# Kernel optimization log

Measured on AMD Instinct MI355X. Metric: run time of the kernel, lower is better.

The kernel has to match this reference:

```python
import jax, jax.numpy as jnp
import numpy as np

BIT = 64
NUM_TRAIN = 100000
N_CLASS = 100
BATCH = 128
MU = 1.0
NU = 0.1
ETA = 55.0
DCC_ITER = 10


def setup_inputs() -> dict:
    key = jax.random.key(0)
    k1, k2, k3, k4, k5 = jax.random.split(key, 5)
    u = jax.random.normal(k1, (BATCH, BIT), dtype=jnp.float32)
    y = (jax.random.uniform(k2, (BATCH, N_CLASS)) < 0.1).astype(jnp.float32)
    ind = jnp.arange(BATCH, dtype=jnp.int32)  # unique column indices into num_train
    U = jax.random.normal(k3, (BIT, NUM_TRAIN), dtype=jnp.float32)
    B = jnp.sign(jax.random.normal(k4, (BIT, NUM_TRAIN), dtype=jnp.float32))  # +-1 codes
    Ybuf = (jax.random.uniform(k5, (N_CLASS, NUM_TRAIN)) < 0.1).astype(jnp.float32)
    return {"u": u, "y": y, "ind": ind, "U": U, "B": B, "Ybuf": Ybuf}


def _update_b_and_w(B, U, Ybuf):
    # Faithful DCC: dcc_iter outer iterations; within each, W from a ridge
    # solve, then sequential sign coordinate-descent over the `bit` rows of B.
    lam_eye = (NU / MU) * jnp.eye(BIT, dtype=B.dtype)
    W = None
    for _ in range(DCC_ITER):
        # W = inv(B B^T + (nu/mu) I) @ B @ Y^T  -> (bit, n_class)
        W = jnp.linalg.solve(B @ B.T + lam_eye, B @ Ybuf.T)
        P = W @ Ybuf + (ETA / MU) * U  # (bit, num_train); constant within inner loop

        def body(Bc, i):
            w = W[i]                         # (n_class,)
            Ww = W @ w                       # (bit,)
            # B_prime.T @ W_prime @ w == B.T @ (W @ w) - B[i] * (w . w)
            row = jnp.sign(P[i] - (Ww @ Bc - Bc[i] * (w @ w)))
            return Bc.at[i].set(row), None

        B, _ = jax.lax.scan(body, B, jnp.arange(BIT))
    return B, W


def reference(u, y, ind, U, B, Ybuf):
    # buffer updates: U gets detached u (torch uses u.t().data), Y gets y
    U = U.at[:, ind].set(jax.lax.stop_gradient(u).T)
    Ybuf = Ybuf.at[:, ind].set(y.T)
    B, W = _update_b_and_w(B, U, Ybuf)

    inner_product = (u @ U) * 0.5                       # (batch, num_train)
    s = (y @ Ybuf > 0).astype(u.dtype)                  # (batch, num_train)
    likelihood = jnp.log1p(jnp.exp(-jnp.abs(inner_product))) \
        + jnp.maximum(inner_product, 0.0) - s * inner_product
    likelihood_loss = jnp.mean(likelihood)
    cl_loss = jnp.mean((y.T - W.T @ B[:, ind]) ** 2)    # (n_class, batch)
    reg_loss = jnp.mean(W ** 2)
    return likelihood_loss + MU * cl_loss + NU * reg_loss
```

## Files before the change

kernel.cpp:

```cpp
#include <hip/hip_runtime.h>
#include <cstdint>
#include <cstddef>


#define NT 100000
#define WPR 1568
#define NWREAL 1563
#define NGRPP 1568
#define NJB 1563
#define ETA_MU 55.0f
#define LAM 0.1f

typedef unsigned long long u64;
typedef _Float16 half8 __attribute__((ext_vector_type(8)));
typedef _Float16 half4 __attribute__((ext_vector_type(4)));
typedef _Float16 half2v __attribute__((ext_vector_type(2)));
typedef float float4v __attribute__((ext_vector_type(4)));

__device__ inline float hsum8(half8 a) {
  half4 lo = __builtin_shufflevector(a, a, 0, 1, 2, 3);
  half4 hi = __builtin_shufflevector(a, a, 4, 5, 6, 7);
  half4 s4 = lo + hi;
  half2v l2 = __builtin_shufflevector(s4, s4, 0, 1);
  half2v h2 = __builtin_shufflevector(s4, s4, 2, 3);
  half2v s2 = l2 + h2;
  return (float)s2[0] + (float)s2[1];
}

__device__ inline u64 transpose64(u64 x, int lane) {
  const u64 ms[6] = {0x5555555555555555ull,0x3333333333333333ull,0x0F0F0F0F0F0F0F0Full,
                     0x00FF00FF00FF00FFull,0x0000FFFF0000FFFFull,0x00000000FFFFFFFFull};
#pragma unroll
  for (int si = 0; si < 6; ++si) {
    int s = 1 << si;
    u64 m = ms[si];
    u64 y = __shfl_xor(x, s, 64);
    if ((lane & s) == 0) x = (x & m) | ((y & m) << s);
    else                 x = (x & ~m) | ((y & ~m) >> s);
  }
  return x;
}

__device__ inline int wave_reduce_i32(int v) {
#pragma unroll
  for (int off = 32; off > 0; off >>= 1) v += __shfl_down(v, off, 64);
  return v;
}
__device__ inline double wave_reduce_f64(double v) {
#pragma unroll
  for (int off = 32; off > 0; off >>= 1) v += __shfl_down(v, off, 64);
  return v;
}

__global__ __launch_bounds__(256) void build_colmasks(
    const float* __restrict__ B, const float* __restrict__ Ybuf,
    u64* __restrict__ Bmask, u64* __restrict__ Ymask,
    signed char* __restrict__ owner, int* __restrict__ cflags) {
  if (blockIdx.x == 0 && threadIdx.x < 16) cflags[threadIdx.x] = 0;
  int j0 = (blockIdx.x * 256 + threadIdx.x) * 4;
  if (j0 >= NT) return;
  *(int*)&owner[j0] = -1;
  u64 bm[4] = {0, 0, 0, 0};
#pragma unroll
  for (int i = 0; i < 64; ++i) {
    float4 v = *(const float4*)&B[(size_t)i * NT + j0];
    bm[0] |= ((u64)(v.x > 0.0f)) << i;
    bm[1] |= ((u64)(v.y > 0.0f)) << i;
    bm[2] |= ((u64)(v.z > 0.0f)) << i;
    bm[3] |= ((u64)(v.w > 0.0f)) << i;
  }
  u64 m0[4] = {0, 0, 0, 0}, m1[4] = {0, 0, 0, 0};
#pragma unroll
  for (int c = 0; c < 100; ++c) {
    float4 v = *(const float4*)&Ybuf[(size_t)c * NT + j0];
    if (c < 64) {
      m0[0] |= ((u64)(v.x > 0.5f)) << c;
      m0[1] |= ((u64)(v.y > 0.5f)) << c;
      m0[2] |= ((u64)(v.z > 0.5f)) << c;
      m0[3] |= ((u64)(v.w > 0.5f)) << c;
    } else {
      m1[0] |= ((u64)(v.x > 0.5f)) << (c - 64);
      m1[1] |= ((u64)(v.y > 0.5f)) << (c - 64);
      m1[2] |= ((u64)(v.z > 0.5f)) << (c - 64);
      m1[3] |= ((u64)(v.w > 0.5f)) << (c - 64);
    }
  }
#pragma unroll
  for (int t = 0; t < 4; ++t) {
    Bmask[j0 + t] = bm[t];
    Ymask[2 * (j0 + t)] = m0[t];
    Ymask[2 * (j0 + t) + 1] = m1[t];
  }
}

__global__ void scatter_y(const float* __restrict__ y, const int* __restrict__ ind,
                          u64* __restrict__ Ymask, u64* __restrict__ ybatch,
                          signed char* __restrict__ owner) {
  int b = threadIdx.x;
  if (b >= 128) return;
  u64 m0 = 0, m1 = 0;
  for (int c = 0; c < 100; ++c) {
    bool v = y[b * 100 + c] > 0.5f;
    if (c < 64) m0 |= ((u64)v) << c;
    else        m1 |= ((u64)v) << (c - 64);
  }
  ybatch[2 * b] = m0;
  ybatch[2 * b + 1] = m1;
  int col = ind[b];
  Ymask[2 * col] = m0;
  Ymask[2 * col + 1] = m1;
  owner[col] = (signed char)b;
}

__global__ __launch_bounds__(256) void build_rows(
    const u64* __restrict__ Bmask, const u64* __restrict__ Ymask,
    u64* __restrict__ Brow, u64* __restrict__ Yrow) {
  int g = blockIdx.x * 4 + (threadIdx.x >> 6);
  int lane = threadIdx.x & 63;
  if (g >= NGRPP) return;
  int j = g * 64 + lane;
  bool act = j < NT;
  u64 bm = act ? Bmask[j] : 0ull;
  u64 y0 = act ? Ymask[2 * j] : 0ull;
  u64 y1 = act ? Ymask[2 * j + 1] : 0ull;
  u64 tb = transpose64(bm, lane);
  Brow[(size_t)lane * WPR + g] = tb;
  u64 t0 = transpose64(y0, lane);
  Yrow[(size_t)lane * WPR + g] = t0;
  u64 t1 = transpose64(y1, lane);
  if (lane < 36) Yrow[(size_t)(64 + lane) * WPR + g] = t1;
}

__global__ __launch_bounds__(256) void popcY_k(const u64* __restrict__ Yrow,
                                               int* __restrict__ popcY) {
  int c = blockIdx.x;
  __shared__ int red[4];
  int s = 0;
  for (int w = threadIdx.x; w < NWREAL; w += 256)
    s += __popcll(Yrow[(size_t)c * WPR + w]);
  s = wave_reduce_i32(s);
  if ((threadIdx.x & 63) == 0) red[threadIdx.x >> 6] = s;
  __syncthreads();
  if (threadIdx.x == 0) popcY[c] = red[0] + red[1] + red[2] + red[3];
}

__global__ __launch_bounds__(256, 4) void k1_sr(
    const u64* __restrict__ Brow, const u64* __restrict__ Yrow,
    int* __restrict__ S_part, int* __restrict__ R_part,
    int it, const int* __restrict__ cflags) {
  if (it > 0 && cflags[it - 1] == 0) return;
  int k = blockIdx.x;
  int q = blockIdx.y;
  int w0 = q * 196;
  int wv = threadIdx.x >> 6, lane = threadIdx.x & 63;
  u64 tmask = (lane < 4) ? ~0ull : 0ull;
  const u64* bk = Brow + (size_t)k * WPR + w0;
  u64 b0 = bk[lane], b1 = bk[lane + 64], b2 = bk[lane + 128];
  u64 b3 = bk[192 + (lane & 3)] & tmask;
  int sS[16];
#pragma unroll
  for (int m = 0; m < 16; ++m) {
    const u64* br = Brow + (size_t)(4 * m + wv) * WPR + w0;
    u64 x0 = br[lane], x1 = br[lane + 64], x2 = br[lane + 128];
    u64 x3 = br[192 + (lane & 3)] & tmask;
    sS[m] = __popcll(x0 ^ b0) + __popcll(x1 ^ b1) +
            __popcll(x2 ^ b2) + __popcll(x3 ^ b3);
  }
  int sR[25];
#pragma unroll
  for (int m = 0; m < 25; ++m) {
    const u64* yr = Yrow + (size_t)(4 * m + wv) * WPR + w0;
    u64 x0 = yr[lane], x1 = yr[lane + 64], x2 = yr[lane + 128];
    u64 x3 = yr[192 + (lane & 3)] & tmask;
    sR[m] = __popcll(x0 & b0) + __popcll(x1 & b1) +
            __popcll(x2 & b2) + __popcll(x3 & b3);
  }
#pragma unroll
  for (int off = 32; off > 0; off >>= 1) {
#pragma unroll
    for (int m = 0; m < 16; ++m) sS[m] += __shfl_down(sS[m], off, 64);
#pragma unroll
    for (int m = 0; m < 25; ++m) sR[m] += __shfl_down(sR[m], off, 64);
  }
  if (lane == 0) {
#pragma unroll
    for (int m = 0; m < 16; ++m)
      S_part[q * 4096 + k * 64 + 4 * m + wv] = sS[m];
#pragma unroll
    for (int m = 0; m < 25; ++m)
      R_part[q * 6400 + k * 100 + 4 * m + wv] = sR[m];
  }
}

__global__ __launch_bounds__(256, 1) void k2a_solve(
    const int* __restrict__ S_part, const int* __restrict__ R_part,
    const int* __restrict__ popcY, float* __restrict__ Wr,
    float* __restrict__ Wc, int it, const int* __restrict__ cflags) {
  if (it > 0 && cflags[it - 1] == 0) return;
  __shared__ short sEi[4096];
  __shared__ _Float16 sXa[64 * 32];
  __shared__ _Float16 sXb[64 * 32];
  int tid = threadIdx.x;
  int wv = tid >> 6, k = tid & 63;
  int b = blockIdx.x;
  const int qbase_t[4] = {0, 7, 14, 20};
  const int qcnt_t[4]  = {7, 7, 6, 6};
  int qbase = qbase_t[b], Q = qcnt_t[b];
  const int off7[4] = {0, 2, 4, 6}, cnt7[4] = {2, 2, 2, 1};
  const int off6[4] = {0, 2, 4, 5}, cnt6[4] = {2, 2, 1, 1};
  int woff = (Q == 7) ? off7[wv] : off6[wv];
  int wcnt = (Q == 7) ? cnt7[wv] : cnt6[wv];
  const float alpha = 1.0f / (100000.0f + LAM);
  for (int e = tid; e < 4096; e += 256) {
    int kk = e >> 6, ll = e & 63;
    int mm = 0;
#pragma unroll
    for (int qq = 0; qq < 8; ++qq) mm += S_part[qq * 4096 + e];
    int v = (kk == ll) ? 0 : (NT - 2 * mm);
    v = v > 32767 ? 32767 : (v < -32767 ? -32767 : v);
    sEi[kk * 64 + (ll ^ (kk & 31))] = (short)v;
  }
  float4 rr4[2], xf[2];
#pragma unroll
  for (int q = 0; q < 2; ++q) {
    if (q < wcnt) {
      float tmp[4];
#pragma unroll
      for (int e4 = 0; e4 < 4; ++e4) {
        int cg = 4 * (qbase + woff + q) + e4;
        float rv = 0.0f;
        if (cg < 100) {
          int rr = 0;
#pragma unroll
          for (int qq = 0; qq < 8; ++qq) rr += R_part[qq * 6400 + k * 100 + cg];
          rv = (float)(2 * rr - popcY[cg]);
        }
        tmp[e4] = rv;
      }
      rr4[q] = make_float4(tmp[0], tmp[1], tmp[2], tmp[3]);
      xf[q] = make_float4(alpha * tmp[0], alpha * tmp[1],
                          alpha * tmp[2], alpha * tmp[3]);
    }
  }
  if (wcnt == 2) {
    half8 h;
    h[0] = (_Float16)xf[0].x; h[1] = (_Float16)xf[0].y;
    h[2] = (_Float16)xf[0].z; h[3] = (_Float16)xf[0].w;
    h[4] = (_Float16)xf[1].x; h[5] = (_Float16)xf[1].y;
    h[6] = (_Float16)xf[1].z; h[7] = (_Float16)xf[1].w;
    *(half8*)&sXa[k * 32 + 4 * woff] = h;
  } else {
    half4 h;
    h[0] = (_Float16)xf[0].x; h[1] = (_Float16)xf[0].y;
    h[2] = (_Float16)xf[0].z; h[3] = (_Float16)xf[0].w;
    *(half4*)&sXa[k * 32 + 4 * woff] = h;
  }
  __syncthreads();
  _Float16* Xs = sXa;
  _Float16* Xd = sXb;
  for (int it2 = 0; it2 < 4; ++it2) {
    float4 a4[2];
#pragma unroll
    for (int q = 0; q < 2; ++q)
      if (q < wcnt) a4[q] = rr4[q];
    if (wcnt == 2) {
      for (int l = 0; l < 64; ++l) {
        float ev = (float)sEi[k * 64 + (l ^ (k & 31))];
        half8 x8 = *(const half8*)&Xs[l * 32 + 4 * woff];
        a4[0].x -= ev * (float)x8[0]; a4[0].y -= ev * (float)x8[1];
        a4[0].z -= ev * (float)x8[2]; a4[0].w -= ev * (float)x8[3];
        a4[1].x -= ev * (float)x8[4]; a4[1].y -= ev * (float)x8[5];
        a4[1].z -= ev * (float)x8[6]; a4[1].w -= ev * (float)x8[7];
      }
    } else {
      for (int l = 0; l < 64; ++l) {
        float ev = (float)sEi[k * 64 + (l ^ (k & 31))];
        half4 x4 = *(const half4*)&Xs[l * 32 + 4 * woff];
        a4[0].x -= ev * (float)x4[0]; a4[0].y -= ev * (float)x4[1];
        a4[0].z -= ev * (float)x4[2]; a4[0].w -= ev * (float)x4[3];
      }
    }
#pragma unroll
    for (int q = 0; q < 2; ++q) {
      if (q < wcnt) {
        xf[q] = make_float4(alpha * a4[q].x, alpha * a4[q].y,
                            alpha * a4[q].z, alpha * a4[q].w);
      }
    }
    if (it2 < 3) {
      if (wcnt == 2) {
        half8 h;
        h[0] = (_Float16)xf[0].x; h[1] = (_Float16)xf[0].y;
        h[2] = (_Float16)xf[0].z; h[3] = (_Float16)xf[0].w;
        h[4] = (_Float16)xf[1].x; h[5] = (_Float16)xf[1].y;
        h[6] = (_Float16)xf[1].z; h[7] = (_Float16)xf[1].w;
        *(half8*)&Xd[k * 32 + 4 * woff] = h;
      } else {
        half4 h;
        h[0] = (_Float16)xf[0].x; h[1] = (_Float16)xf[0].y;
        h[2] = (_Float16)xf[0].z; h[3] = (_Float16)xf[0].w;
        *(half4*)&Xd[k * 32 + 4 * woff] = h;
      }
      __syncthreads();
      _Float16* t = Xs; Xs = Xd; Xd = t;
    }
  }
#pragma unroll
  for (int q = 0; q < 2; ++q) {
    if (q < wcnt) {
      float v4[4] = {xf[q].x, xf[q].y, xf[q].z, xf[q].w};
#pragma unroll
      for (int e4 = 0; e4 < 4; ++e4) {
        int cg = 4 * (qbase + woff + q) + e4;
        if (cg < 100) {
          Wr[k * 100 + cg] = v4[e4];
          Wc[cg * 64 + k] = v4[e4];
        }
      }
    }
  }
}

__global__ __launch_bounds__(256, 1) void k2b_gram(
    const float* __restrict__ Wr, float* __restrict__ G,
    int it, const int* __restrict__ cflags) {
  if (it > 0 && cflags[it - 1] == 0) return;
  __shared__ float sX[6400];
  int tid = threadIdx.x, wv = tid >> 6, k = tid & 63;
  for (int t = tid; t < 6400; t += 256) sX[t] = Wr[t];
  __syncthreads();
  float4 xl[25];
#pragma unroll
  for (int q = 0; q < 25; ++q) xl[q] = *(const float4*)&sX[k * 100 + 4 * q];
#pragma unroll
  for (int ii = 0; ii < 4; ++ii) {
    int i = blockIdx.x * 16 + wv * 4 + ii;
    const float4* xi = (const float4*)&sX[i * 100];
    float d0 = 0.f, d1 = 0.f, d2 = 0.f, d3 = 0.f;
#pragma unroll
    for (int q = 0; q < 25; ++q) {
      float4 a = xi[q];
      d0 += xl[q].x * a.x; d1 += xl[q].y * a.y;
      d2 += xl[q].z * a.z; d3 += xl[q].w * a.w;
    }
    G[i * 64 + k] = (d0 + d1) + (d2 + d3);
  }
}

__global__ __launch_bounds__(256, 2) void k3_gs(
    const float* __restrict__ U, const float* __restrict__ u,
    const signed char* __restrict__ owner, const float* __restrict__ Wc,
    const float* __restrict__ Gm, u64* __restrict__ Bmask,
    u64* __restrict__ Brow, const u64* __restrict__ Ymask,
    int it, int* __restrict__ cflags) {
  if (it > 0 && cflags[it - 1] == 0) return;
  __shared__ _Float16 sWh[100 * 72];
  __shared__ _Float16 sGh[64 * 64];
  __shared__ float sGd[64];
  for (int t = threadIdx.x; t < 6400; t += 256) {
    int c = t >> 6, i = t & 63;
    sWh[c * 72 + i] = (_Float16)Wc[t];
  }
  for (int t = threadIdx.x; t < 4096; t += 256) sGh[t] = (_Float16)Gm[t];
  if (threadIdx.x < 64) sGd[threadIdx.x] = Gm[threadIdx.x * 65];
  __syncthreads();
  int g = blockIdx.x * 4 + (threadIdx.x >> 6);
  int lane = threadIdx.x & 63;
  int j = g * 64 + lane;
  bool act = j < NT;
  int jc = act ? j : NT - 1;
  int ow = owner[jc];
  float p[64];
  if (ow >= 0) {
#pragma unroll
    for (int i = 0; i < 64; ++i) p[i] = ETA_MU * u[ow * 64 + i];
  } else {
#pragma unroll
    for (int i = 0; i < 64; ++i) p[i] = ETA_MU * U[(size_t)i * NT + jc];
  }
  u64 y0 = Ymask[2 * jc], y1 = Ymask[2 * jc + 1];
  half8 pw[8];
#pragma unroll
  for (int t = 0; t < 8; ++t) pw[t] = (half8)(_Float16)0.0f;
  u64 mm = y0;
  while (mm) {
    int c = __builtin_ctzll(mm); mm &= mm - 1;
    const half8* wr = (const half8*)&sWh[c * 72];
#pragma unroll
    for (int t = 0; t < 8; ++t) pw[t] += wr[t];
  }
  mm = y1;
  while (mm) {
    int c = 64 + __builtin_ctzll(mm); mm &= mm - 1;
    const half8* wr = (const half8*)&sWh[c * 72];
#pragma unroll
    for (int t = 0; t < 8; ++t) pw[t] += wr[t];
  }
#pragma unroll
  for (int t = 0; t < 8; ++t)
#pragma unroll
    for (int e = 0; e < 8; ++e)
      p[8 * t + e] += (float)pw[t][e];
  u64 bm = Bmask[jc];
  half8 bfh[8];
#pragma unroll
  for (int t = 0; t < 8; ++t)
#pragma unroll
    for (int e = 0; e < 8; ++e)
      bfh[t][e] = ((bm >> (8 * t + e)) & 1ull) ? (_Float16)1.0f : (_Float16)-1.0f;
#pragma unroll
  for (int i = 0; i < 64; ++i) {
    const half8* gr = (const half8*)&sGh[i * 64];
    half8 d = gr[0] * bfh[0];
#pragma unroll
    for (int t = 1; t < 8; ++t) d += gr[t] * bfh[t];
    float dot = hsum8(d);
    float bfi = (float)bfh[i >> 3][i & 7];
    float val = p[i] - dot + sGd[i] * bfi;
    bfh[i >> 3][i & 7] = (val > 0.0f) ? (_Float16)1.0f : (_Float16)-1.0f;
  }
  u64 nm = 0;
#pragma unroll
  for (int t = 0; t < 8; ++t)
#pragma unroll
    for (int e = 0; e < 8; ++e)
      if (bfh[t][e] > (_Float16)0.0f) nm |= 1ull << (8 * t + e);
  if (!act) nm = 0;
  bool ch = act && (nm != bm);
  if (__any(ch) && lane == 0) cflags[it] = 1;
  if (act) Bmask[j] = nm;
  u64 tb = transpose64(nm, lane);
  Brow[(size_t)lane * WPR + g] = tb;
}

__global__ __launch_bounds__(256, 4) void l1_like(
    const float* __restrict__ U, const float* __restrict__ u,
    const signed char* __restrict__ owner, const u64* __restrict__ Ymask,
    const u64* __restrict__ ybatch, double* __restrict__ partial) {
  __shared__ _Float16 shu[8192];
  __shared__ u64 sy[256];
  __shared__ double wred[4];
  int tid = threadIdx.x;
  for (int e = tid; e < 1024; e += 256) {
    int b = e >> 3, k8 = e & 7;
    const float4* src = (const float4*)&u[b * 64 + k8 * 8];
    float4 f0 = src[0], f1 = src[1];
    half8 h;
    h[0] = (_Float16)f0.x; h[1] = (_Float16)f0.y;
    h[2] = (_Float16)f0.z; h[3] = (_Float16)f0.w;
    h[4] = (_Float16)f1.x; h[5] = (_Float16)f1.y;
    h[6] = (_Float16)f1.z; h[7] = (_Float16)f1.w;
    *(half8*)&shu[b * 64 + ((k8 ^ (b & 7)) * 8)] = h;
  }
  if (tid < 256) sy[tid] = ybatch[tid];
  __syncthreads();
  int wv = tid >> 6, lane = tid & 63;
  int n = lane & 15, q = lane >> 4;
  int j = blockIdx.x * 64 + wv * 16 + n;
  bool actj = j < NT;
  int jc = actj ? j : NT - 1;
  int ow = owner[jc];
  half8 bf0, bf1;
#pragma unroll
  for (int t = 0; t < 8; ++t) {
    int k = q * 8 + t;
    bf0[t] = (_Float16)U[(size_t)k * NT + jc];
    bf1[t] = (_Float16)U[(size_t)(k + 32) * NT + jc];
  }
  if (ow >= 0) {
#pragma unroll
    for (int t = 0; t < 8; ++t) {
      bf0[t] = (_Float16)u[ow * 64 + q * 8 + t];
      bf1[t] = (_Float16)u[ow * 64 + 32 + q * 8 + t];
    }
  }
  u64 ym0 = Ymask[2 * jc], ym1 = Ymask[2 * jc + 1];
  float lsum = 0.0f;
#pragma unroll
  for (int t8 = 0; t8 < 8; ++t8) {
    int brow = t8 * 16 + n;
    half8 a0 = *(const half8*)&shu[brow * 64 + ((q ^ (brow & 7)) * 8)];
    half8 a1 = *(const half8*)&shu[brow * 64 + (((q + 4) ^ (brow & 7)) * 8)];
    float4v c = {0.f, 0.f, 0.f, 0.f};
    c = __builtin_amdgcn_mfma_f32_16x16x32_f16(a0, bf0, c, 0, 0, 0);
    c = __builtin_amdgcn_mfma_f32_16x16x32_f16(a1, bf1, c, 0, 0, 0);
#pragma unroll
    for (int r = 0; r < 4; ++r) {
      int b = t8 * 16 + q * 4 + r;
      float ip = 0.5f * c[r];
      u64 yb0 = sy[2 * b], yb1 = sy[2 * b + 1];
      bool s = ((yb0 & ym0) | (yb1 & ym1)) != 0ull;
      float a = fabsf(ip);
      lsum += __logf(1.0f + __expf(-a)) + fmaxf(ip, 0.0f) - (s ? ip : 0.0f);
    }
  }
  if (!actj) lsum = 0.0f;
  double lsd = wave_reduce_f64((double)lsum);
  if (lane == 0) wred[wv] = lsd;
  __syncthreads();
  if (tid == 0)
    partial[blockIdx.x] = wred[0] + wred[1] + wred[2] + wred[3];
}

__global__ __launch_bounds__(256) void l2_fin(
    const float* __restrict__ Wr, const float* __restrict__ y,
    const int* __restrict__ ind, const u64* __restrict__ Bmask,
    const double* __restrict__ partial, float* __restrict__ out) {
  __shared__ float sw[6400];
  __shared__ u64 sbm[128];
  __shared__ double dred[12];
  int tid = threadIdx.x;
  for (int t = tid; t < 6400; t += 256) sw[t] = Wr[t];
  if (tid < 128) sbm[tid] = Bmask[ind[tid]];
  __syncthreads();
  double cls = 0.0, regs = 0.0, l1s = 0.0;
  for (int e = tid; e < 12800; e += 256) {
    int c = e >> 7, b = e & 127;
    u64 bm = sbm[b];
    float s = 0.0f;
#pragma unroll
    for (int i = 0; i < 64; ++i) {
      float w = sw[i * 100 + c];
      s += ((bm >> i) & 1ull) ? w : -w;
    }
    float d = y[b * 100 + c] - s;
    cls += (double)(d * d);
  }
  for (int e = tid; e < 6400; e += 256) {
    float w = sw[e];
    regs += (double)(w * w);
  }
  for (int t = tid; t < NJB; t += 256) l1s += partial[t];
  cls = wave_reduce_f64(cls);
  regs = wave_reduce_f64(regs);
  l1s = wave_reduce_f64(l1s);
  int wv = tid >> 6;
  if ((tid & 63) == 0) { dred[wv] = cls; dred[4 + wv] = regs; dred[8 + wv] = l1s; }
  __syncthreads();
  if (tid == 0) {
    double c = dred[0] + dred[1] + dred[2] + dred[3];
    double r = dred[4] + dred[5] + dred[6] + dred[7];
    double l = dred[8] + dred[9] + dred[10] + dred[11];
    out[0] = (float)(l * (1.0 / 12800000.0) + c * (1.0 / 12800.0) +
                     r * (0.1 / 6400.0));
  }
}

extern "C" void kernel_launch(void* const* d_in, const int* in_sizes, int n_in,
                              void* d_out, int out_size, void* d_ws, size_t ws_size,
                              hipStream_t stream) {
  const float* u    = (const float*)d_in[0];
  const float* y    = (const float*)d_in[1];
  const int*   ind  = (const int*)d_in[2];
  const float* U    = (const float*)d_in[3];
  const float* B    = (const float*)d_in[4];
  const float* Ybuf = (const float*)d_in[5];
  char* ws = (char*)d_ws;
  int* cflags        = (int*)ws;
  u64* Bmask         = (u64*)(ws + 256);
  u64* Ymask         = (u64*)(ws + 800256);
  u64* Brow          = (u64*)(ws + 2400256);
  u64* Yrow          = (u64*)(ws + 3203072);
  u64* ybatch        = (u64*)(ws + 4457472);
  int* popcY         = (int*)(ws + 4459520);
  int* S_part        = (int*)(ws + 4460032);
  int* R_part        = (int*)(ws + 4591104);
  float* Wr          = (float*)(ws + 4795904);
  float* Wc          = (float*)(ws + 4821504);
  float* G           = (float*)(ws + 4847104);
  signed char* owner = (signed char*)(ws + 4863488);
  double* partial    = (double*)(ws + 4963520);

  build_colmasks<<<98, 256, 0, stream>>>(B, Ybuf, Bmask, Ymask, owner, cflags);
  scatter_y<<<1, 128, 0, stream>>>(y, ind, Ymask, ybatch, owner);
  build_rows<<<392, 256, 0, stream>>>(Bmask, Ymask, Brow, Yrow);
  popcY_k<<<100, 256, 0, stream>>>(Yrow, popcY);
  for (int it = 0; it < 10; ++it) {
    k1_sr<<<dim3(64, 8), 256, 0, stream>>>(Brow, Yrow, S_part, R_part, it, cflags);
    k2a_solve<<<4, 256, 0, stream>>>(S_part, R_part, popcY, Wr, Wc, it, cflags);
    k2b_gram<<<4, 256, 0, stream>>>(Wr, G, it, cflags);
    k3_gs<<<392, 256, 0, stream>>>(U, u, owner, Wc, G, Bmask, Brow, Ymask, it, cflags);
  }
  l1_like<<<NJB, 256, 0, stream>>>(U, u, owner, Ymask, ybatch, partial);
  l2_fin<<<1, 256, 0, stream>>>(Wr, y, ind, Bmask, partial, (float*)d_out);
}
```

Baseline: 577.9 us.

## Incrementally update Gauss-Seidel residuals, fuse popcount into row build, widen mask grid

The per-column sign coordinate descent in k3_gs now precomputes G·b once. After that, each row flip applies a rank-1 correction only when some lane in the wave changes sign, instead of recomputing a full 64-wide dot product for every row. The Y popcount kernel is removed and its counts are accumulated with atomics inside build_rows, with popcY zeroed in scatter_y. build_colmasks now runs one column per thread over 391 blocks instead of four columns per thread over 98 blocks, giving more parallelism but scalar loads. Accumulating the running residual in fp16 could drift slightly from the previous per-row recomputation.

```diff
diff --git a/kernel.cpp b/kernel.cpp
--- a/kernel.cpp
+++ b/kernel.cpp
@@ -57,47 +57,31 @@
     u64* __restrict__ Bmask, u64* __restrict__ Ymask,
     signed char* __restrict__ owner, int* __restrict__ cflags) {
   if (blockIdx.x == 0 && threadIdx.x < 16) cflags[threadIdx.x] = 0;
-  int j0 = (blockIdx.x * 256 + threadIdx.x) * 4;
-  if (j0 >= NT) return;
-  *(int*)&owner[j0] = -1;
-  u64 bm[4] = {0, 0, 0, 0};
-#pragma unroll
-  for (int i = 0; i < 64; ++i) {
-    float4 v = *(const float4*)&B[(size_t)i * NT + j0];
-    bm[0] |= ((u64)(v.x > 0.0f)) << i;
-    bm[1] |= ((u64)(v.y > 0.0f)) << i;
-    bm[2] |= ((u64)(v.z > 0.0f)) << i;
-    bm[3] |= ((u64)(v.w > 0.0f)) << i;
-  }
-  u64 m0[4] = {0, 0, 0, 0}, m1[4] = {0, 0, 0, 0};
-#pragma unroll
-  for (int c = 0; c < 100; ++c) {
-    float4 v = *(const float4*)&Ybuf[(size_t)c * NT + j0];
-    if (c < 64) {
-      m0[0] |= ((u64)(v.x > 0.5f)) << c;
-      m0[1] |= ((u64)(v.y > 0.5f)) << c;
-      m0[2] |= ((u64)(v.z > 0.5f)) << c;
-      m0[3] |= ((u64)(v.w > 0.5f)) << c;
-    } else {
-      m1[0] |= ((u64)(v.x > 0.5f)) << (c - 64);
-      m1[1] |= ((u64)(v.y > 0.5f)) << (c - 64);
-      m1[2] |= ((u64)(v.z > 0.5f)) << (c - 64);
-      m1[3] |= ((u64)(v.w > 0.5f)) << (c - 64);
-    }
-  }
-#pragma unroll
-  for (int t = 0; t < 4; ++t) {
-    Bmask[j0 + t] = bm[t];
-    Ymask[2 * (j0 + t)] = m0[t];
-    Ymask[2 * (j0 + t) + 1] = m1[t];
-  }
+  int j = blockIdx.x * 256 + threadIdx.x;
+  if (j >= NT) return;
+  owner[j] = (signed char)-1;
+  u64 bm = 0;
+#pragma unroll
+  for (int i = 0; i < 64; ++i)
+    bm |= ((u64)(B[(size_t)i * NT + j] > 0.0f)) << i;
+  u64 m0 = 0, m1 = 0;
+#pragma unroll
+  for (int c = 0; c < 64; ++c)
+    m0 |= ((u64)(Ybuf[(size_t)c * NT + j] > 0.5f)) << c;
+#pragma unroll
+  for (int c = 64; c < 100; ++c)
+    m1 |= ((u64)(Ybuf[(size_t)c * NT + j] > 0.5f)) << (c - 64);
+  Bmask[j] = bm;
+  Ymask[2 * j] = m0;
+  Ymask[2 * j + 1] = m1;
 }
 
 __global__ void scatter_y(const float* __restrict__ y, const int* __restrict__ ind,
                           u64* __restrict__ Ymask, u64* __restrict__ ybatch,
-                          signed char* __restrict__ owner) {
+                          signed char* __restrict__ owner, int* __restrict__ popcY) {
   int b = threadIdx.x;
   if (b >= 128) return;
+  if (b < 100) popcY[b] = 0;
   u64 m0 = 0, m1 = 0;
   for (int c = 0; c < 100; ++c) {
     bool v = y[b * 100 + c] > 0.5f;
@@ -114,7 +98,7 @@
 
 __global__ __launch_bounds__(256) void build_rows(
     const u64* __restrict__ Bmask, const u64* __restrict__ Ymask,
-    u64* __restrict__ Brow, u64* __restrict__ Yrow) {
+    u64* __restrict__ Brow, u64* __restrict__ Yrow, int* __restrict__ popcY) {
   int g = blockIdx.x * 4 + (threadIdx.x >> 6);
   int lane = threadIdx.x & 63;
   if (g >= NGRPP) return;
@@ -127,21 +111,12 @@
   Brow[(size_t)lane * WPR + g] = tb;
   u64 t0 = transpose64(y0, lane);
   Yrow[(size_t)lane * WPR + g] = t0;
+  atomicAdd(&popcY[lane], (int)__popcll(t0));
   u64 t1 = transpose64(y1, lane);
-  if (lane < 36) Yrow[(size_t)(64 + lane) * WPR + g] = t1;
-}
-
-__global__ __launch_bounds__(256) void popcY_k(const u64* __restrict__ Yrow,
-                                               int* __restrict__ popcY) {
-  int c = blockIdx.x;
-  __shared__ int red[4];
-  int s = 0;
-  for (int w = threadIdx.x; w < NWREAL; w += 256)
-    s += __popcll(Yrow[(size_t)c * WPR + w]);
-  s = wave_reduce_i32(s);
-  if ((threadIdx.x & 63) == 0) red[threadIdx.x >> 6] = s;
-  __syncthreads();
-  if (threadIdx.x == 0) popcY[c] = red[0] + red[1] + red[2] + red[3];
+  if (lane < 36) {
+    Yrow[(size_t)(64 + lane) * WPR + g] = t1;
+    atomicAdd(&popcY[64 + lane], (int)__popcll(t1));
+  }
 }
 
 __global__ __launch_bounds__(256, 4) void k1_sr(
@@ -408,16 +383,29 @@
 #pragma unroll
     for (int e = 0; e < 8; ++e)
       bfh[t][e] = ((bm >> (8 * t + e)) & 1ull) ? (_Float16)1.0f : (_Float16)-1.0f;
+  half8 qv[8];
+#pragma unroll
+  for (int t = 0; t < 8; ++t) qv[t] = (half8)(_Float16)0.0f;
 #pragma unroll
   for (int i = 0; i < 64; ++i) {
     const half8* gr = (const half8*)&sGh[i * 64];
-    half8 d = gr[0] * bfh[0];
-#pragma unroll
-    for (int t = 1; t < 8; ++t) d += gr[t] * bfh[t];
-    float dot = hsum8(d);
-    float bfi = (float)bfh[i >> 3][i & 7];
-    float val = p[i] - dot + sGd[i] * bfi;
-    bfh[i >> 3][i & 7] = (val > 0.0f) ? (_Float16)1.0f : (_Float16)-1.0f;
+    _Float16 bi = bfh[i >> 3][i & 7];
+#pragma unroll
+    for (int t = 0; t < 8; ++t) qv[t] += gr[t] * bi;
+  }
+#pragma unroll
+  for (int i = 0; i < 64; ++i) {
+    _Float16 ob = bfh[i >> 3][i & 7];
+    float val = p[i] - (float)qv[i >> 3][i & 7] + sGd[i] * (float)ob;
+    _Float16 nb = (val > 0.0f) ? (_Float16)1.0f : (_Float16)-1.0f;
+    bool ch = (nb != ob);
+    if (__any(ch)) {
+      _Float16 dl = ch ? (_Float16)(nb + nb) : (_Float16)0.0f;
+      const half8* gr = (const half8*)&sGh[i * 64];
+#pragma unroll
+      for (int t = 0; t < 8; ++t) qv[t] += gr[t] * dl;
+      bfh[i >> 3][i & 7] = nb;
+    }
   }
   u64 nm = 0;
 #pragma unroll
@@ -571,10 +559,9 @@
   signed char* owner = (signed char*)(ws + 4863488);
   double* partial    = (double*)(ws + 4963520);
 
-  build_colmasks<<<98, 256, 0, stream>>>(B, Ybuf, Bmask, Ymask, owner, cflags);
-  scatter_y<<<1, 128, 0, stream>>>(y, ind, Ymask, ybatch, owner);
-  build_rows<<<392, 256, 0, stream>>>(Bmask, Ymask, Brow, Yrow);
-  popcY_k<<<100, 256, 0, stream>>>(Yrow, popcY);
+  build_colmasks<<<391, 256, 0, stream>>>(B, Ybuf, Bmask, Ymask, owner, cflags);
+  scatter_y<<<1, 128, 0, stream>>>(y, ind, Ymask, ybatch, owner, popcY);
+  build_rows<<<392, 256, 0, stream>>>(Bmask, Ymask, Brow, Yrow, popcY);
   for (int it = 0; it < 10; ++it) {
     k1_sr<<<dim3(64, 8), 256, 0, stream>>>(Brow, Yrow, S_part, R_part, it, cflags);
     k2a_solve<<<4, 256, 0, stream>>>(S_part, R_part, popcY, Wr, Wc, it, cflags);
```

After: 588.5 us. About the same (+1.8%).
